# Optimization experiments

Hardware: AMD Instinct MI355X
Metric: run time of the kernel (lower is better)

Reference implementation:

```python
import jax, jax.numpy as jnp
import numpy as np

TIME_GAP_BUCKETS = 64
B, L, H, MAX_T = 256, 200, 256, 256
VOCAB, N_GROUPS = 50000, 16
EPS = 1e-5


def setup_inputs() -> dict:
    key = jax.random.key(0)
    ks = jax.random.split(key, 16)
    lengths = jax.random.randint(ks[0], (B,), 0, L + 1)
    mask = jnp.arange(L)[None, :] < lengths[:, None]

    def toks(k, hi):  # jagged padded-dense: zeros past each row's length
        return jnp.where(mask, jax.random.randint(k, (B, L), 0, hi), 0)

    inp = {
        'history_tokens': toks(ks[1], VOCAB),
        'history_post_tokens': toks(ks[2], VOCAB),
        'history_author_tokens': toks(ks[3], VOCAB),
        'history_action_tokens': toks(ks[4], VOCAB),
        'history_time_gap': toks(ks[5], TIME_GAP_BUCKETS + 1),
        'history_group_ids': jnp.where(mask, jnp.sort(jax.random.randint(ks[6], (B, L), 1, N_GROUPS + 1), axis=1), 0),
        'lengths': lengths,
    }
    s = 0.02
    inp['token_emb'] = jax.random.normal(ks[7], (VOCAB, H)) * s
    inp['ln_gamma'] = jnp.ones((6 * H,))
    inp['ln_beta'] = jnp.zeros((6 * H,))
    inp['w1'] = jax.random.normal(ks[8], (6 * H, 4 * H)) * (1.0 / np.sqrt(6 * H)).astype(np.float32)
    inp['b1'] = jnp.zeros((4 * H,))
    inp['w2'] = jax.random.normal(ks[9], (4 * H, H)) * (1.0 / np.sqrt(4 * H)).astype(np.float32)
    inp['b2'] = jnp.zeros((H,))
    inp['time_gap_emb'] = (jax.random.normal(ks[10], (TIME_GAP_BUCKETS + 1, H)) * s).at[0].set(0.0)  # padding_idx=0
    inp['group_emb'] = (jax.random.normal(ks[11], (N_GROUPS + 1, H)) * s).at[0].set(0.0)  # padding_idx=0
    inp['pos_emb'] = jax.random.normal(ks[12], (MAX_T, H)) * s
    inp['sep_token'] = jax.random.normal(ks[13], (H,)) * 0.02
    return inp


def _layernorm(x, g, b):
    mu = jnp.mean(x, axis=-1, keepdims=True)
    var = jnp.mean(jnp.square(x - mu), axis=-1, keepdims=True)
    return (x - mu) * jax.lax.rsqrt(var + EPS) * g + b


def _merge_with_sep(event_tokens, group_ids, mask, sep_token):
    # mask is a prefix mask (positions < lengths), so valid tokens are contiguous.
    Bn, Ln, Hn = event_tokens.shape
    next_mask = jnp.pad(mask[:, 1:], ((0, 0), (0, 1)))
    next_group = jnp.pad(group_ids[:, 1:], ((0, 0), (0, 1)))
    sep_after = mask & next_mask & (group_ids != next_group)  # insert sep after token i
    seps_before = jnp.cumsum(sep_after, axis=1) - sep_after.astype(jnp.int32)  # exclusive scan
    token_pos = jnp.arange(Ln)[None, :] + seps_before  # position within merged piece list
    total = mask.sum(axis=1) + sep_after.sum(axis=1)  # [B] merged piece count
    offset = MAX_T - total  # right-align; negative -> leading pieces dropped
    tok_idx = offset[:, None] + token_pos
    sep_idx = tok_idx + 1
    tok_idx = jnp.where(mask & (tok_idx >= 0), tok_idx, MAX_T)  # MAX_T => dropped
    sep_idx = jnp.where(sep_after & (sep_idx >= 0), sep_idx, MAX_T)
    sep_rows = jnp.broadcast_to(sep_token, (Ln, Hn))

    def scatter_one(ev, ti, si):
        buf = jnp.zeros((MAX_T, Hn), ev.dtype)
        buf = buf.at[ti].set(ev, mode='drop')
        buf = buf.at[si].set(sep_rows, mode='drop')
        return buf

    merged = jax.vmap(scatter_one)(event_tokens, tok_idx, sep_idx)
    merged_len = jnp.minimum(total, MAX_T)
    merged_mask = jnp.arange(MAX_T)[None, :] >= (MAX_T - merged_len)[:, None]
    return merged, merged_mask


def reference(history_tokens, history_post_tokens, history_author_tokens,
              history_action_tokens, history_time_gap, history_group_ids,
              lengths, token_emb, ln_gamma, ln_beta, w1, b1, w2, b2,
              time_gap_emb, group_emb, pos_emb, sep_token):
    mask = jnp.arange(L)[None, :] < lengths[:, None]
    hh = token_emb[history_tokens]
    ph = token_emb[history_post_tokens]
    ah = token_emb[history_author_tokens]
    ch = token_emb[history_action_tokens]
    th = time_gap_emb[jnp.clip(history_time_gap, 0, TIME_GAP_BUCKETS)]
    gh = group_emb[history_group_ids]
    ev = jnp.concatenate([hh, ph, ah, ch, th, gh], axis=-1)  # [B, L, 6H]
    x = _layernorm(ev, ln_gamma, ln_beta)
    x = jax.nn.silu(x @ w1 + b1)  # dropout is identity in eval mode
    event_tokens = x @ w2 + b2  # [B, L, H]
    merged, mm = _merge_with_sep(event_tokens, history_group_ids, mask, sep_token)
    merged = (merged + pos_emb[None]) * mm[..., None].astype(merged.dtype)
    return merged, mm
```

## Files before the change

### kernel.cpp

```cpp
#include <hip/hip_runtime.h>
#include <hip/hip_bf16.h>
#include <math.h>

#define B_    256
#define L_    200
#define H_    256
#define MAXT  256
#define SIXH  1536
#define FOURH 1024
#define NPOS  (B_ * L_)

typedef __attribute__((ext_vector_type(8))) short short8;
typedef __attribute__((ext_vector_type(4))) float f32x4;

typedef __attribute__((address_space(3))) void lds_void;
typedef const __attribute__((address_space(1))) void gbl_void;

#define ASM_BAR() asm volatile("s_barrier" ::: "memory")
#define VMCNT4()  asm volatile("s_waitcnt vmcnt(4)" ::: "memory")
#define VMCNT0()  asm volatile("s_waitcnt vmcnt(0)" ::: "memory")

__global__ void scan_offsets(const int* __restrict__ lengths,
                             int* __restrict__ offsets) {
  if (threadIdx.x == 0) {
    int acc = 0;
    for (int b = 0; b < B_; b++) { offsets[b] = acc; acc += lengths[b]; }
    offsets[B_] = acc;
  }
}

__global__ void zero_pad_x(__hip_bfloat16* __restrict__ x,
                           const int* __restrict__ offsets) {
  int total = offsets[B_];
  int padded = (total + 255) & ~255;
  int row = total + blockIdx.x;
  if (row >= padded) return;
  int t = threadIdx.x;
#pragma unroll
  for (int j = 0; j < 6; j++)
    x[(size_t)row * SIXH + j * 256 + t] = __float2bfloat16(0.0f);
}

__global__ void tpos_kernel(const int* __restrict__ gids,
                            const int* __restrict__ lengths,
                            const int* __restrict__ offsets,
                            int* __restrict__ tpos) {
  int b = blockIdx.x, t = threadIdx.x;
  __shared__ int g[L_];
  int len = lengths[b];
  for (int l = t; l < len; l += 64) g[l] = gids[b * L_ + l];
  __syncthreads();
  if (t != 0) return;
  int base = offsets[b];
  int nsep = 0;
  for (int l = 0; l + 1 < len; l++)
    if (g[l] != g[l + 1]) nsep++;
  int total = len + nsep;
  int off = MAXT - total;
  int sb = 0;
  for (int l = 0; l < len; l++) {
    int ti = off + l + sb;
    tpos[base + l] = (ti >= 0) ? (b * MAXT + ti) : -1;
    if (l + 1 < len && g[l] != g[l + 1]) sb++;
  }
}

__global__ void transpose_to_bf16(const float* __restrict__ in,
                                  __hip_bfloat16* __restrict__ out,
                                  int R, int C) {
  __shared__ float tile[32][33];
  int tc = blockIdx.x, tr = blockIdx.y;
  int tx = threadIdx.x & 31, ty = threadIdx.x >> 5;
#pragma unroll
  for (int i = 0; i < 4; i++) {
    int r = tr * 32 + ty + i * 8;
    int c = tc * 32 + tx;
    tile[ty + i * 8][tx] = in[(size_t)r * C + c];
  }
  __syncthreads();
#pragma unroll
  for (int i = 0; i < 4; i++) {
    int orow = tc * 32 + ty + i * 8;
    int ocol = tr * 32 + tx;
    out[(size_t)orow * R + ocol] = __float2bfloat16(tile[tx][ty + i * 8]);
  }
}

__global__ void embed_ln_kernel(const int* __restrict__ tok0,
                                const int* __restrict__ tok1,
                                const int* __restrict__ tok2,
                                const int* __restrict__ tok3,
                                const int* __restrict__ tgap,
                                const int* __restrict__ gid,
                                const int* __restrict__ lengths,
                                const int* __restrict__ offsets,
                                const float* __restrict__ token_emb,
                                const float* __restrict__ tg_emb,
                                const float* __restrict__ g_emb,
                                const float* __restrict__ gamma,
                                const float* __restrict__ beta,
                                __hip_bfloat16* __restrict__ xout) {
  int l = blockIdx.x, b = blockIdx.y;
  if (l >= lengths[b]) return;
  int pos = b * L_ + l;
  int row = offsets[b] + l;
  int t = threadIdx.x;
  int wv = t >> 6;
  int ln = t & 63;
  int c4 = ln * 4;

  const float* tab;
  int idx;
  if (wv == 0)      { tab = token_emb; idx = tok0[pos]; }
  else if (wv == 1) { tab = token_emb; idx = tok1[pos]; }
  else if (wv == 2) { tab = token_emb; idx = tok2[pos]; }
  else if (wv == 3) { tab = token_emb; idx = tok3[pos]; }
  else if (wv == 4) { tab = tg_emb;    idx = min(max(tgap[pos], 0), 64); }
  else              { tab = g_emb;     idx = gid[pos]; }

  float4 v = *(const float4*)&tab[(size_t)idx * H_ + c4];

  float s = v.x + v.y + v.z + v.w;
  float q = v.x * v.x + v.y * v.y + v.z * v.z + v.w * v.w;
#pragma unroll
  for (int o = 32; o; o >>= 1) { s += __shfl_down(s, o); q += __shfl_down(q, o); }
  __shared__ float ps[6], pq[6];
  if (ln == 0) { ps[wv] = s; pq[wv] = q; }
  __syncthreads();
  float ts = 0.f, tq = 0.f;
#pragma unroll
  for (int k = 0; k < 6; k++) { ts += ps[k]; tq += pq[k]; }
  float mu = ts * (1.0f / 1536.0f);
  float var = tq * (1.0f / 1536.0f) - mu * mu;
  float rstd = rsqrtf(var + 1e-5f);

  int cbase = wv * 256 + c4;
  float4 gm = *(const float4*)&gamma[cbase];
  float4 bt = *(const float4*)&beta[cbase];
  float y0 = (v.x - mu) * rstd * gm.x + bt.x;
  float y1 = (v.y - mu) * rstd * gm.y + bt.y;
  float y2 = (v.z - mu) * rstd * gm.z + bt.z;
  float y3 = (v.w - mu) * rstd * gm.w + bt.w;
  __hip_bfloat16 h0 = __float2bfloat16(y0), h1 = __float2bfloat16(y1);
  __hip_bfloat16 h2 = __float2bfloat16(y2), h3 = __float2bfloat16(y3);
  ushort4 pk;
  pk.x = *(unsigned short*)&h0; pk.y = *(unsigned short*)&h1;
  pk.z = *(unsigned short*)&h2; pk.w = *(unsigned short*)&h3;
  *(ushort4*)&xout[(size_t)row * SIXH + cbase] = pk;
}

__global__ __launch_bounds__(512, 2)
void gemm1_8ph(const __hip_bfloat16* __restrict__ A,
               const __hip_bfloat16* __restrict__ Bt,
               const float* __restrict__ bias,
               __hip_bfloat16* __restrict__ out,
               const int* __restrict__ total_ptr) {
  constexpr int K = SIXH;
  constexpr int NT = K / 64;
  constexpr int N = FOURH;

  extern __shared__ __align__(16) char lds[];

  int total = total_ptr[0];
  int padded = (total + 255) & ~255;
  int num_mt = padded >> 8;

  int bid = blockIdx.x;
  int nt = (bid & 7) >> 1;
  int local = ((bid >> 3) << 1) | (bid & 1);
  int n0 = nt * 256;

  int tid = threadIdx.x;
  int lane = tid & 63;
  int w = tid >> 6;
  int wave_m = w >> 2;
  int wave_n = w & 3;

  int r15 = lane & 15, g = lane >> 4;
  int slot_r = (((r15 & 1) << 2) | g) ^ (r15 >> 1);
  int lane_off = (r15 >> 1) * 128 + slot_r * 16;

  int s0 = (tid & 7) ^ ((tid >> 3) & 7);
  int scol = (s0 & 3) * 8;
  int row0 = ((tid >> 3) << 1) + (s0 >> 2);
  int ldst0 = w * 1024;

  float bv4[4];
#pragma unroll
  for (int ni = 0; ni < 4; ni++)
    bv4[ni] = bias[n0 + wave_n * 64 + ni * 16 + r15];

#define REGA(d, h) (lds + (d) * 65536 + (h) * 16384)
#define REGB(d, h) (lds + (d) * 65536 + 32768 + (h) * 16384)

#define STAGE(P, t0, kt, h, rb)                                                \
  do {                                                                         \
    __builtin_amdgcn_global_load_lds(                                          \
        (gbl_void*)((P) + (size_t)((t0) + row0) * K + (kt) * 64 + (h) * 32 +   \
                    scol),                                                     \
        (lds_void*)((rb) + ldst0), 16, 0, 0);                                  \
    __builtin_amdgcn_global_load_lds(                                          \
        (gbl_void*)((P) + (size_t)((t0) + row0 + 128) * K + (kt) * 64 +        \
                    (h) * 32 + scol),                                          \
        (lds_void*)((rb) + 8192 + ldst0), 16, 0, 0);                           \
  } while (0)

  for (int mt = local; mt < num_mt; mt += 64) {
    int m0 = mt * 256;

    f32x4 acc[8][4] = {};

    STAGE(A, m0, 0, 0, REGA(0, 0));
    STAGE(Bt, n0, 0, 0, REGB(0, 0));
    STAGE(A, m0, 0, 1, REGA(0, 1));
    STAGE(Bt, n0, 0, 1, REGB(0, 1));
    STAGE(A, m0, 1, 0, REGA(1, 0));
    STAGE(Bt, n0, 1, 0, REGB(1, 0));
    VMCNT4();
    ASM_BAR();

    for (int kt = 0; kt < NT; ++kt) {
      int d = kt & 1;
      int kc1 = (kt + 1 < NT) ? kt + 1 : NT - 1;
      int kc2 = (kt + 2 < NT) ? kt + 2 : NT - 1;
      char* A0 = REGA(d, 0); char* A1 = REGA(d, 1);
      char* B0 = REGB(d, 0); char* B1 = REGB(d, 1);
      char* An1 = REGA(d ^ 1, 1);
      char* Bn1 = REGB(d ^ 1, 1);

      short8 a[4], b[4];

#pragma unroll
      for (int ni = 0; ni < 4; ni++)
        b[ni] = *(const short8*)(B0 + (wave_n * 64 + ni * 16) * 64 + lane_off);
#pragma unroll
      for (int j = 0; j < 4; j++)
        a[j] = *(const short8*)(A0 + (wave_m * 128 + j * 16) * 64 + lane_off);
      STAGE(A, m0, kc1, 1, An1);
      ASM_BAR();
      __builtin_amdgcn_s_setprio(1);
#pragma unroll
      for (int j = 0; j < 4; j++)
#pragma unroll
        for (int ni = 0; ni < 4; ni++)
          acc[j][ni] = __builtin_amdgcn_mfma_f32_16x16x32_bf16(a[j], b[ni],
                                                               acc[j][ni], 0, 0, 0);
      __builtin_amdgcn_s_setprio(0);
      ASM_BAR();

#pragma unroll
      for (int j = 0; j < 4; j++)
        a[j] = *(const short8*)(A0 + (wave_m * 128 + (4 + j) * 16) * 64 + lane_off);
      STAGE(Bt, n0, kc1, 1, Bn1);
      ASM_BAR();
      __builtin_amdgcn_s_setprio(1);
#pragma unroll
      for (int j = 0; j < 4; j++)
#pragma unroll
        for (int ni = 0; ni < 4; ni++)
          acc[4 + j][ni] = __builtin_amdgcn_mfma_f32_16x16x32_bf16(
              a[j], b[ni], acc[4 + j][ni], 0, 0, 0);
      __builtin_amdgcn_s_setprio(0);
      ASM_BAR();

#pragma unroll
      for (int ni = 0; ni < 4; ni++)
        b[ni] = *(const short8*)(B1 + (wave_n * 64 + ni * 16) * 64 + lane_off);
#pragma unroll
      for (int j = 0; j < 4; j++)
        a[j] = *(const short8*)(A1 + (wave_m * 128 + j * 16) * 64 + lane_off);
      STAGE(A, m0, kc2, 0, A0);
      ASM_BAR();
      __builtin_amdgcn_s_setprio(1);
#pragma unroll
      for (int j = 0; j < 4; j++)
#pragma unroll
        for (int ni = 0; ni < 4; ni++)
          acc[j][ni] = __builtin_amdgcn_mfma_f32_16x16x32_bf16(a[j], b[ni],
                                                               acc[j][ni], 0, 0, 0);
      __builtin_amdgcn_s_setprio(0);
      ASM_BAR();

#pragma unroll
      for (int j = 0; j < 4; j++)
        a[j] = *(const short8*)(A1 + (wave_m * 128 + (4 + j) * 16) * 64 + lane_off);
      STAGE(Bt, n0, kc2, 0, B0);
      ASM_BAR();
      __builtin_amdgcn_s_setprio(1);
#pragma unroll
      for (int j = 0; j < 4; j++)
#pragma unroll
        for (int ni = 0; ni < 4; ni++)
          acc[4 + j][ni] = __builtin_amdgcn_mfma_f32_16x16x32_bf16(
              a[j], b[ni], acc[4 + j][ni], 0, 0, 0);
      __builtin_amdgcn_s_setprio(0);
      VMCNT4();
      ASM_BAR();
    }
    VMCNT0();

    int r0 = g * 4;
#pragma unroll
    for (int mi = 0; mi < 8; mi++)
#pragma unroll
      for (int ni = 0; ni < 4; ni++) {
        int col = n0 + wave_n * 64 + ni * 16 + r15;
        float bv = bv4[ni];
#pragma unroll
        for (int r = 0; r < 4; r++) {
          int row = m0 + wave_m * 128 + mi * 16 + r0 + r;
          float v = acc[mi][ni][r] + bv;
          v = v / (1.0f + __expf(-v));
          out[(size_t)row * N + col] = __float2bfloat16(v);
        }
      }
  }
#undef STAGE
#undef REGA
#undef REGB
}

__global__ void gemm2_scatter(const __hip_bfloat16* __restrict__ A,
                              const __hip_bfloat16* __restrict__ Bt,
                              const float* __restrict__ bias,
                              const int* __restrict__ tpos,
                              const float* __restrict__ pos_emb,
                              float* __restrict__ out,
                              const int* __restrict__ total_ptr,
                              int N, int K) {
  int m0 = blockIdx.y * 128;
  int total = total_ptr[0];
  int padded = (total + 127) & ~127;
  if (m0 >= padded) return;

  __shared__ __hip_bfloat16 As[128 * 64];
  __shared__ __hip_bfloat16 Bs[128 * 64];
  int n0 = blockIdx.x * 128;
  int tid = threadIdx.x;
  int lane = tid & 63, wid = tid >> 6;
  int wm = (wid >> 1) * 64, wn = (wid & 1) * 64;

  int srow = (lane >> 3);
  int scol = (lane & 7) * 8;

  f32x4 acc[4][4] = {};

  for (int k0 = 0; k0 < K; k0 += 64) {
#pragma unroll
    for (int i = 0; i < 4; i++) {
      int c = wid * 4 + i;
      int row = c * 8 + srow;
      __builtin_amdgcn_global_load_lds(
          (gbl_void*)&A[(size_t)(m0 + row) * K + k0 + scol],
          (lds_void*)(As + c * 512), 16, 0, 0);
      __builtin_amdgcn_global_load_lds(
          (gbl_void*)&Bt[(size_t)(n0 + row) * K + k0 + scol],
          (lds_void*)(Bs + c * 512), 16, 0, 0);
    }
    __syncthreads();
#pragma unroll
    for (int kk = 0; kk < 64; kk += 32) {
      short8 a[4], bb[4];
#pragma unroll
      for (int m = 0; m < 4; m++)
        a[m] = *(const short8*)&As[(wm + m * 16 + (lane & 15)) * 64 + kk +
                                   8 * (lane >> 4)];
#pragma unroll
      for (int n = 0; n < 4; n++)
        bb[n] = *(const short8*)&Bs[(wn + n * 16 + (lane & 15)) * 64 + kk +
                                    8 * (lane >> 4)];
#pragma unroll
      for (int m = 0; m < 4; m++)
#pragma unroll
        for (int n = 0; n < 4; n++)
          acc[m][n] = __builtin_amdgcn_mfma_f32_16x16x32_bf16(a[m], bb[n],
                                                              acc[m][n], 0, 0, 0);
    }
    __syncthreads();
  }

  int r0 = (lane >> 4) * 4;
  int cc = lane & 15;
#pragma unroll
  for (int m = 0; m < 4; m++) {
#pragma unroll
    for (int r = 0; r < 4; r++) {
      int row = m0 + wm + m * 16 + r0 + r;
      if (row >= total) continue;
      int pa = tpos[row];
      if (pa < 0) continue;
      int p = pa & (MAXT - 1);
#pragma unroll
      for (int n = 0; n < 4; n++) {
        int col = n0 + wn + n * 16 + cc;
        float v = acc[m][n][r] + bias[col] + pos_emb[p * H_ + col];
        out[(size_t)pa * H_ + col] = v;
      }
    }
  }
}

__global__ void merge2_kernel(const int* __restrict__ gids,
                              const int* __restrict__ lengths,
                              const float* __restrict__ sep_token,
                              const float* __restrict__ pos_emb,
                              float* __restrict__ out) {
  int b = blockIdx.x, t = threadIdx.x;
  __shared__ signed char src[MAXT];
  __shared__ int g[L_];
  __shared__ int sh_total;
  int len = lengths[b];
  src[t] = 0;
  for (int l = t; l < len; l += 256) g[l] = gids[b * L_ + l];
  __syncthreads();
  if (t == 0) {
    int nsep = 0;
    for (int l = 0; l + 1 < len; l++)
      if (g[l] != g[l + 1]) nsep++;
    int total = len + nsep;
    sh_total = total;
    int off = MAXT - total;
    int sb = 0;
    for (int l = 0; l < len; l++) {
      int ti = off + l + sb;
      if (ti >= 0) src[ti] = 2;
      if (l + 1 < len && g[l] != g[l + 1]) {
        if (ti + 1 >= 0) src[ti + 1] = 1;
        sb++;
      }
    }
  }
  __syncthreads();
  int total = sh_total;
  int mlen = min(total, MAXT);

  int q = t >> 6, lane = t & 63, c4 = lane * 4;
  float4 sep4 = *(const float4*)&sep_token[c4];
  float* orow = out + (size_t)b * MAXT * H_;
  for (int p0 = 0; p0 < MAXT; p0 += 4) {
    int p = p0 + q;
    int s = src[p];
    if (s == 2) continue;
    float4 v;
    if (s == 1) {
      float4 pe = *(const float4*)&pos_emb[p * H_ + c4];
      v.x = sep4.x + pe.x; v.y = sep4.y + pe.y;
      v.z = sep4.z + pe.z; v.w = sep4.w + pe.w;
    } else {
      v.x = 0.f; v.y = 0.f; v.z = 0.f; v.w = 0.f;
    }
    *(float4*)&orow[(size_t)p * H_ + c4] = v;
  }
  float* mm = out + (size_t)B_ * MAXT * H_;
  mm[b * MAXT + t] = (t >= MAXT - mlen) ? 1.0f : 0.0f;
}

extern "C" void kernel_launch(void* const* d_in, const int* in_sizes, int n_in,
                              void* d_out, int out_size, void* d_ws,
                              size_t ws_size, hipStream_t stream) {
  const int* tok0 = (const int*)d_in[0];
  const int* tok1 = (const int*)d_in[1];
  const int* tok2 = (const int*)d_in[2];
  const int* tok3 = (const int*)d_in[3];
  const int* tgap = (const int*)d_in[4];
  const int* gid  = (const int*)d_in[5];
  const int* lengths = (const int*)d_in[6];
  const float* token_emb = (const float*)d_in[7];
  const float* gamma = (const float*)d_in[8];
  const float* beta  = (const float*)d_in[9];
  const float* w1 = (const float*)d_in[10];
  const float* b1 = (const float*)d_in[11];
  const float* w2 = (const float*)d_in[12];
  const float* b2 = (const float*)d_in[13];
  const float* tg_emb = (const float*)d_in[14];
  const float* g_emb  = (const float*)d_in[15];
  const float* pos_emb = (const float*)d_in[16];
  const float* sep_tok = (const float*)d_in[17];

  const size_t NEEDED = 265815044;
  if (ws_size < NEEDED) return;

  char* ws = (char*)d_ws;
  __hip_bfloat16* x = (__hip_bfloat16*)ws;
  int* tpos = (int*)ws;
  __hip_bfloat16* h = (__hip_bfloat16*)(ws + 157286400);
  __hip_bfloat16* w1t = (__hip_bfloat16*)(ws + 262144000);
  __hip_bfloat16* w2t = (__hip_bfloat16*)(ws + 265289728);
  int* offsets = (int*)(ws + 265814016);

  scan_offsets<<<1, 64, 0, stream>>>(lengths, offsets);
  zero_pad_x<<<256, 256, 0, stream>>>(x, offsets);

  transpose_to_bf16<<<dim3(1024 / 32, 1536 / 32), 256, 0, stream>>>(w1, w1t,
                                                                    1536, 1024);
  transpose_to_bf16<<<dim3(256 / 32, 1024 / 32), 256, 0, stream>>>(w2, w2t,
                                                                   1024, 256);

  embed_ln_kernel<<<dim3(L_, B_), 384, 0, stream>>>(
      tok0, tok1, tok2, tok3, tgap, gid, lengths, offsets, token_emb, tg_emb,
      g_emb, gamma, beta, x);

  hipFuncSetAttribute((const void*)gemm1_8ph,
                      hipFuncAttributeMaxDynamicSharedMemorySize, 131072);
  gemm1_8ph<<<256, 512, 131072, stream>>>(x, w1t, b1, h, offsets + B_);

  tpos_kernel<<<B_, 64, 0, stream>>>(gid, lengths, offsets, tpos);

  gemm2_scatter<<<dim3(H_ / 128, NPOS / 128), 256, 0, stream>>>(
      h, w2t, b2, tpos, pos_emb, (float*)d_out, offsets + B_, H_, FOURH);

  merge2_kernel<<<B_, 256, 0, stream>>>(gid, lengths, sep_tok, pos_emb,
                                        (float*)d_out);
}
```

Measured before the change: 259.1 us.

## Widen gemm2 tile to full N and remap gemm1 blocks across XCDs

gemm2 now has each block compute a 128x256 tile covering the whole output width, which doubles per-wave accumulators to 4x8. The A tile is therefore loaded once per row block instead of twice, at the cost of more registers and LDS per block. gemm1's block-to-tile mapping changes so that blocks on the same XCD share the same M tile across the four N tiles, aiming to improve L2 reuse of A.

```diff
diff --git a/kernel.cpp b/kernel.cpp
--- a/kernel.cpp
+++ b/kernel.cpp
@@ -166,8 +166,10 @@
   int num_mt = padded >> 8;
 
   int bid = blockIdx.x;
-  int nt = (bid & 7) >> 1;
-  int local = ((bid >> 3) << 1) | (bid & 1);
+  int xcd = bid & 7;
+  int slot = bid >> 3;
+  int nt = slot & 3;
+  int mtb = slot >> 2;
   int n0 = nt * 256;
 
   int tid = threadIdx.x;
@@ -205,7 +207,7 @@
         (lds_void*)((rb) + 8192 + ldst0), 16, 0, 0);                           \
   } while (0)
 
-  for (int mt = local; mt < num_mt; mt += 64) {
+  for (int mt = xcd + 8 * mtb; mt < num_mt; mt += 64) {
     int m0 = mt * 256;
 
     f32x4 acc[8][4] = {};
@@ -326,24 +328,25 @@
                               const int* __restrict__ tpos,
                               const float* __restrict__ pos_emb,
                               float* __restrict__ out,
-                              const int* __restrict__ total_ptr,
-                              int N, int K) {
-  int m0 = blockIdx.y * 128;
+                              const int* __restrict__ total_ptr) {
+  constexpr int K = FOURH;
+  int m0 = blockIdx.x * 128;
   int total = total_ptr[0];
   int padded = (total + 127) & ~127;
   if (m0 >= padded) return;
 
   __shared__ __hip_bfloat16 As[128 * 64];
-  __shared__ __hip_bfloat16 Bs[128 * 64];
-  int n0 = blockIdx.x * 128;
+  __shared__ __hip_bfloat16 Bs[256 * 64];
   int tid = threadIdx.x;
   int lane = tid & 63, wid = tid >> 6;
-  int wm = (wid >> 1) * 64, wn = (wid & 1) * 64;
+  int wm = (wid >> 1) * 64;
+  int wn = (wid & 1) * 128;
 
   int srow = (lane >> 3);
   int scol = (lane & 7) * 8;
-
-  f32x4 acc[4][4] = {};
+  int r15 = lane & 15, g = lane >> 4;
+
+  f32x4 acc[4][8] = {};
 
   for (int k0 = 0; k0 < K; k0 += 64) {
 #pragma unroll
@@ -353,34 +356,36 @@
       __builtin_amdgcn_global_load_lds(
           (gbl_void*)&A[(size_t)(m0 + row) * K + k0 + scol],
           (lds_void*)(As + c * 512), 16, 0, 0);
+    }
+#pragma unroll
+    for (int i = 0; i < 8; i++) {
+      int c = wid * 8 + i;
+      int row = c * 8 + srow;
       __builtin_amdgcn_global_load_lds(
-          (gbl_void*)&Bt[(size_t)(n0 + row) * K + k0 + scol],
+          (gbl_void*)&Bt[(size_t)row * K + k0 + scol],
           (lds_void*)(Bs + c * 512), 16, 0, 0);
     }
     __syncthreads();
 #pragma unroll
     for (int kk = 0; kk < 64; kk += 32) {
-      short8 a[4], bb[4];
+      short8 a[4], bb[8];
 #pragma unroll
       for (int m = 0; m < 4; m++)
-        a[m] = *(const short8*)&As[(wm + m * 16 + (lane & 15)) * 64 + kk +
-                                   8 * (lane >> 4)];
-#pragma unroll
-      for (int n = 0; n < 4; n++)
-        bb[n] = *(const short8*)&Bs[(wn + n * 16 + (lane & 15)) * 64 + kk +
-                                    8 * (lane >> 4)];
+        a[m] = *(const short8*)&As[(wm + m * 16 + r15) * 64 + kk + 8 * g];
+#pragma unroll
+      for (int n = 0; n < 8; n++)
+        bb[n] = *(const short8*)&Bs[(wn + n * 16 + r15) * 64 + kk + 8 * g];
 #pragma unroll
       for (int m = 0; m < 4; m++)
 #pragma unroll
-        for (int n = 0; n < 4; n++)
+        for (int n = 0; n < 8; n++)
           acc[m][n] = __builtin_amdgcn_mfma_f32_16x16x32_bf16(a[m], bb[n],
                                                               acc[m][n], 0, 0, 0);
     }
     __syncthreads();
   }
 
-  int r0 = (lane >> 4) * 4;
-  int cc = lane & 15;
+  int r0 = g * 4;
 #pragma unroll
   for (int m = 0; m < 4; m++) {
 #pragma unroll
@@ -391,8 +396,8 @@
       if (pa < 0) continue;
       int p = pa & (MAXT - 1);
 #pragma unroll
-      for (int n = 0; n < 4; n++) {
-        int col = n0 + wn + n * 16 + cc;
+      for (int n = 0; n < 8; n++) {
+        int col = wn + n * 16 + r15;
         float v = acc[m][n][r] + bias[col] + pos_emb[p * H_ + col];
         out[(size_t)pa * H_ + col] = v;
       }
@@ -506,8 +511,8 @@
 
   tpos_kernel<<<B_, 64, 0, stream>>>(gid, lengths, offsets, tpos);
 
-  gemm2_scatter<<<dim3(H_ / 128, NPOS / 128), 256, 0, stream>>>(
-      h, w2t, b2, tpos, pos_emb, (float*)d_out, offsets + B_, H_, FOURH);
+  gemm2_scatter<<<NPOS / 128, 256, 0, stream>>>(h, w2t, b2, tpos, pos_emb,
+                                                (float*)d_out, offsets + B_);
 
   merge2_kernel<<<B_, 256, 0, stream>>>(gid, lengths, sep_tok, pos_emb,
                                         (float*)d_out);
```

Measured after the change: 420.7 us. 1.62x slower.
